# Kernel optimization log

Hardware: AMD Instinct MI355X
Metric: run time of the kernel (lower is better)

Reference implementation:

```python
import jax, jax.numpy as jnp
import numpy as np

B, L, D, H = 8, 1024, 512, 8
DH = D // H
DF = 2048


def setup_inputs() -> dict:
    key = jax.random.key(0)
    ks = jax.random.split(key, 13)
    s = 0.02
    return {
        "hid": jax.random.normal(ks[0], (B, L, D), jnp.float32),
        "img": jax.random.normal(ks[1], (B, L, D), jnp.float32),
        "Wq": s * jax.random.normal(ks[2], (D, D), jnp.float32),
        "Wk": s * jax.random.normal(ks[3], (D, D), jnp.float32),
        "Wv": s * jax.random.normal(ks[4], (D, D), jnp.float32),
        "Wo": s * jax.random.normal(ks[5], (D, D), jnp.float32),
        "Wq2": s * jax.random.normal(ks[6], (D, D), jnp.float32),
        "Wk2": s * jax.random.normal(ks[7], (D, D), jnp.float32),
        "Wv2": s * jax.random.normal(ks[8], (D, D), jnp.float32),
        "Wo2": s * jax.random.normal(ks[9], (D, D), jnp.float32),
        "W1": s * jax.random.normal(ks[10], (D, DF), jnp.float32),
        "W2": s * jax.random.normal(ks[11], (DF, D), jnp.float32),
        "seq": jax.random.randint(ks[12], (B, L), 0, 4),
        "SOC": 3,
        "EOS": 100,
    }


def _ln(x):
    mu = x.mean(-1, keepdims=True)
    v = x.var(-1, keepdims=True)
    return (x - mu) * jax.lax.rsqrt(v + 1e-5)


def _attn(q_in, k_in, v_in, Wq, Wk, Wv, Wo, key_mask=None):
    b, lq, _ = q_in.shape
    q = (q_in @ Wq).reshape(b, lq, H, DH)
    k = (k_in @ Wk).reshape(b, -1, H, DH)
    v = (v_in @ Wv).reshape(b, -1, H, DH)
    scores = jnp.einsum('bqhd,bkhd->bhqk', q, k) * (1.0 / np.sqrt(DH))
    if key_mask is not None:
        scores = jnp.where(key_mask[:, None, None, :], scores, jnp.float32(-1e9))
    a = jax.nn.softmax(scores, axis=-1)
    o = jnp.einsum('bhqk,bkhd->bqhd', a, v).reshape(b, lq, D)
    return o @ Wo


def reference(hid, img, Wq, Wk, Wv, Wo, Wq2, Wk2, Wv2, Wo2, W1, W2, seq, SOC, EOS):
    # cell-start mask: SOC tokens before the first EOS
    soc = (seq == SOC) & (jnp.cumsum(seq == EOS, axis=1) == 0)  # [B,L]
    # stable compaction: True positions first, original order preserved
    order = jnp.argsort(~soc, axis=1, stable=True)              # [B,L]
    ext = jnp.take_along_axis(hid, order[:, :, None], axis=1)   # [B,L,D]
    counts = soc.sum(axis=1)                                    # [B]
    run = jnp.arange(L)[None, :] < counts[:, None]              # [B,L] = extract(soc, soc)
    ext = jnp.where(run[:, :, None], ext, 0.0)                  # zero padding rows (F.pad)
    # Blocks: pre-LN masked self-attn + cross-attn to img + FFN
    x = ext
    xn = _ln(x)
    x = x + _attn(xn, xn, xn, Wq, Wk, Wv, Wo, key_mask=run)
    x = x + _attn(_ln(x), img, img, Wq2, Wk2, Wv2, Wo2)
    x = x + jax.nn.gelu(_ln(x) @ W1) @ W2
    # masked_scatter: write the first `count` rows of x back at soc positions, in order
    inv = jnp.argsort(order, axis=1)
    back = jnp.take_along_axis(x, inv[:, :, None], axis=1)
    hid_new = jnp.where(soc[:, :, None], back, hid)
    return (hid_new, x)
```

## Files before the change

### kernel.cpp

```cpp
#include <hip/hip_runtime.h>
#include <cmath>

#define B 8
#define L 1024
#define D 512
#define H 8
#define DH 64
#define DF 2048
#define BLD (B*L*D)
#define M_TOT (B*L)

typedef __attribute__((ext_vector_type(8))) short bf16x8;
typedef __attribute__((ext_vector_type(4))) float f32x4;
typedef const __attribute__((address_space(1))) void* gas_ptr;
typedef __attribute__((address_space(3))) void* las_ptr;

__device__ __forceinline__ unsigned short f2bf(float f) {
    unsigned int u = __builtin_bit_cast(unsigned int, f);
    u += 0x7FFFu + ((u >> 16) & 1u);
    return (unsigned short)(u >> 16);
}
__device__ __forceinline__ float bf2f(unsigned short s) {
    return __builtin_bit_cast(float, ((unsigned int)s) << 16);
}

__device__ __forceinline__ float gelu_f(float x) {
    float x3 = x * x * x;
    return 0.5f * x * (1.0f + tanhf(0.7978845608028654f * (x + 0.044715f * x3)));
}

__global__ __launch_bounds__(1024) void pos_kernel(const int* __restrict__ seq,
                                                   const int* __restrict__ pSOC,
                                                   const int* __restrict__ pEOS,
                                                   int* __restrict__ pos,
                                                   int* __restrict__ inv,
                                                   int* __restrict__ counts) {
    int b = blockIdx.x, t = threadIdx.x;
    int lane = t & 63, w = t >> 6;
    int sv = seq[b * L + t];
    int SOC = pSOC[0], EOS = pEOS[0];
    int eosf = (sv == EOS) ? 1 : 0;
    unsigned long long em = __ballot(eosf);
    int eexcl = __popcll(em & ((1ull << lane) - 1ull));
    __shared__ int ewt[16], swt[16];
    if (lane == 63) ewt[w] = eexcl + eosf;
    __syncthreads();
    int ebase = 0;
    for (int i = 0; i < w; ++i) ebase += ewt[i];
    int ecum_incl = ebase + eexcl + eosf;
    int socf = (sv == SOC && ecum_incl == 0) ? 1 : 0;
    unsigned long long sm = __ballot(socf);
    int sexcl = __popcll(sm & ((1ull << lane) - 1ull));
    if (lane == 63) swt[w] = sexcl + socf;
    __syncthreads();
    int sbase = 0, stot = 0;
    for (int i = 0; i < 16; ++i) { int v = swt[i]; if (i < w) sbase += v; stot += v; }
    int rank = sbase + sexcl;
    if (socf) pos[b * L + rank] = t;
    inv[b * L + t] = socf ? rank : -1;
    if (t == 0) counts[b] = stot;
}

__global__ void gather_ln(const float* __restrict__ hid, const int* __restrict__ pos,
                          const int* __restrict__ counts,
                          float* __restrict__ X, unsigned short* __restrict__ Y) {
    int j = blockIdx.x % L, b = blockIdx.x / L;
    int cnt = counts[b];
    if ((j & ~127) > cnt) return;
    int t = threadIdx.x;
    float a = 0.f, b2 = 0.f;
    if (j < cnt) {
        const float* src = hid + (size_t)(b * L + pos[b * L + j]) * D;
        a = src[t]; b2 = src[t + 256];
    }
    size_t row = (size_t)(b * L + j);
    X[row * D + t] = a;
    X[row * D + t + 256] = b2;
    float s = a + b2, sq = a * a + b2 * b2;
    for (int m = 1; m < 64; m <<= 1) {
        s += __shfl_xor(s, m);
        sq += __shfl_xor(sq, m);
    }
    __shared__ float ws[4], wq[4];
    int wid = t >> 6;
    if ((t & 63) == 0) { ws[wid] = s; wq[wid] = sq; }
    __syncthreads();
    s = ws[0] + ws[1] + ws[2] + ws[3];
    sq = wq[0] + wq[1] + wq[2] + wq[3];
    float mu = s * (1.0f / D);
    float var = sq * (1.0f / D) - mu * mu;
    float rs = rsqrtf(var + 1e-5f);
    Y[row * D + t] = f2bf((a - mu) * rs);
    Y[row * D + t + 256] = f2bf((b2 - mu) * rs);
}

__global__ void epilogue_kernel(const float* __restrict__ x, const float* __restrict__ hid,
                                const int* __restrict__ inv, const int* __restrict__ counts,
                                float* __restrict__ out0, float* __restrict__ out1) {
    int l = blockIdx.x % L, b = blockIdx.x / L;
    int t = threadIdx.x;
    int cnt = counts[b];
    int r = inv[b * L + l];
    const float4* s0 = (const float4*)((r >= 0 ? x + (size_t)(b * L + r) * D
                                               : hid + (size_t)(b * L + l) * D));
    ((float4*)(out0 + (size_t)(b * L + l) * D))[t] = s0[t];
    int jsrc = l < cnt ? l : cnt;
    const float4* s1 = (const float4*)(x + (size_t)(b * L + jsrc) * D);
    ((float4*)(out1 + (size_t)(b * L + l) * D))[t] = s1[t];
}

__global__ void ln_kernel(const float* __restrict__ X, unsigned short* __restrict__ Y,
                          const int* __restrict__ counts) {
    int row = blockIdx.x;
    if ((row & 1023 & ~127) > counts[row >> 10]) return;
    int t = threadIdx.x;
    const float* xr = X + (size_t)row * D;
    float a = xr[t], b2 = xr[t + 256];
    float s = a + b2, sq = a * a + b2 * b2;
    for (int m = 1; m < 64; m <<= 1) {
        s += __shfl_xor(s, m);
        sq += __shfl_xor(sq, m);
    }
    __shared__ float ws[4], wq[4];
    int wid = t >> 6;
    if ((t & 63) == 0) { ws[wid] = s; wq[wid] = sq; }
    __syncthreads();
    s = ws[0] + ws[1] + ws[2] + ws[3];
    sq = wq[0] + wq[1] + wq[2] + wq[3];
    float mu = s * (1.0f / D);
    float var = sq * (1.0f / D) - mu * mu;
    float rs = rsqrtf(var + 1e-5f);
    Y[(size_t)row * D + t] = f2bf((a - mu) * rs);
    Y[(size_t)row * D + t + 256] = f2bf((b2 - mu) * rs);
}

struct WtArgs {
    const float* src[10];
    unsigned short* dst[10];
    const float* img;
    unsigned short* imgb;
};
__global__ void wtrans_cvt_all(WtArgs a) {
    int bid = blockIdx.x;
    int tx = threadIdx.x, ty = threadIdx.y;
    if (bid >= 4096) {
        int t = ty * 32 + tx;
        int i = (bid - 4096) * 256 + t;
        float4 f = ((const float4*)a.img)[i];
        ushort4 u;
        u.x = f2bf(f.x); u.y = f2bf(f.y); u.z = f2bf(f.z); u.w = f2bf(f.w);
        ((ushort4*)a.imgb)[i] = u;
        return;
    }
    __shared__ float t[32][33];
    int w, tn, tk, K, N;
    if (bid < 2048)      { w = bid >> 8;      int t2 = bid & 255;  N = 512;  K = 512;  tn = t2 & 15; tk = t2 >> 4; }
    else if (bid < 3072) { w = 8;             int t2 = bid - 2048; N = 2048; K = 512;  tn = t2 & 63; tk = t2 >> 6; }
    else                 { w = 9;             int t2 = bid - 3072; N = 512;  K = 2048; tn = t2 & 15; tk = t2 >> 4; }
    const float* W = a.src[w];
    unsigned short* Wt = a.dst[w];
    int k0 = tk * 32, n0 = tn * 32;
    for (int i = ty; i < 32; i += 8)
        t[i][tx] = W[(size_t)(k0 + i) * N + n0 + tx];
    __syncthreads();
    for (int i = ty; i < 32; i += 8)
        Wt[(size_t)(n0 + i) * K + k0 + tx] = f2bf(t[tx][i]);
}

template<bool SKIP>
__global__ __launch_bounds__(256) void vtrans_kernel(const unsigned short* __restrict__ V,
                                                     int vstride,
                                                     unsigned short* __restrict__ Vt,
                                                     const int* __restrict__ counts) {
    __shared__ unsigned short t[64][72];
    int l0 = (blockIdx.x & 15) * 64;
    int h = (blockIdx.x >> 4) & 7;
    int b = blockIdx.x >> 7;
    if (SKIP && l0 > counts[b]) return;
    int tid = threadIdx.x;
    const unsigned short* vb = V + (size_t)b * L * vstride + h * DH;
    for (int e = tid; e < 512; e += 256) {
        int i = e >> 3, d0 = (e & 7) * 8;
        *(bf16x8*)&t[i][d0] = *(const bf16x8*)&vb[(size_t)(l0 + i) * vstride + d0];
    }
    __syncthreads();
    for (int e = tid; e < 512; e += 256) {
        int d = e & 63, i0 = (e >> 6) * 8;
        bf16x8 val;
        #pragma unroll
        for (int j = 0; j < 8; ++j) val[j] = t[i0 + j][d];
        *(bf16x8*)&Vt[((size_t)((b * H + h) * DH + d)) * L + l0 + i0] = val;
    }
}

template<int MODE, bool SKIP, int S>
__global__ __launch_bounds__(256) void gemm_mfma(const unsigned short* __restrict__ A,
                                                 const unsigned short* __restrict__ Wt,
                                                 void* __restrict__ Cv,
                                                 int K, int N,
                                                 const int* __restrict__ counts) {
    int m0 = blockIdx.y * 64, n0 = blockIdx.x * 128;
    if (SKIP && (m0 & 1023) > counts[m0 >> 10]) return;
    int Kc = K / S;
    int kbeg = blockIdx.z * Kc;
    int nk = Kc / 64;
    __shared__ __align__(16) unsigned short As[3][64 * 64];
    __shared__ __align__(16) unsigned short Bs[3][128 * 64];
    int tid = threadIdx.x, lane = tid & 63, wid = tid >> 6;
    int wm = (wid >> 1) * 32, wn = (wid & 1) * 64;
    int r16 = lane & 15, g = lane >> 4;
    f32x4 acc[2][4] = {};

#define STAGE(bufi, kt) do {                                                          \
    int kk_ = kbeg + (kt) * 64;                                                       \
    _Pragma("unroll")                                                                 \
    for (int q_ = 0; q_ < 2; ++q_) {                                                  \
        int e_ = q_ * 256 + tid;                                                      \
        int r_ = e_ >> 3, c_ = ((e_ & 7) ^ (r_ & 7)) * 8;                             \
        __builtin_amdgcn_global_load_lds((gas_ptr)(A + (size_t)(m0 + r_) * K + kk_ + c_), \
                                         (las_ptr)(&As[bufi][0] + (size_t)e_ * 8), 16, 0, 0); \
    }                                                                                 \
    _Pragma("unroll")                                                                 \
    for (int q_ = 0; q_ < 4; ++q_) {                                                  \
        int e_ = q_ * 256 + tid;                                                      \
        int r_ = e_ >> 3, c_ = ((e_ & 7) ^ (r_ & 7)) * 8;                             \
        __builtin_amdgcn_global_load_lds((gas_ptr)(Wt + (size_t)(n0 + r_) * K + kk_ + c_), \
                                         (las_ptr)(&Bs[bufi][0] + (size_t)e_ * 8), 16, 0, 0); \
    }                                                                                 \
} while (0)

    STAGE(0, 0);
    if (nk > 1) STAGE(1, 1);
    asm volatile("s_waitcnt vmcnt(6)" ::: "memory");
    __builtin_amdgcn_s_barrier();
    __builtin_amdgcn_sched_barrier(0);
    int swz = (r16 & 7) * 8;
    for (int kt = 0; kt < nk; ++kt) {
        int cur = kt % 3;
        if (kt + 2 < nk) STAGE((kt + 2) % 3, kt + 2);
        #pragma unroll
        for (int ks = 0; ks < 2; ++ks) {
            bf16x8 av[2], bv[4];
            #pragma unroll
            for (int m = 0; m < 2; ++m)
                av[m] = *(const bf16x8*)&As[cur][(wm + m * 16 + r16) * 64 + ((ks * 32 + g * 8) ^ swz)];
            #pragma unroll
            for (int n = 0; n < 4; ++n)
                bv[n] = *(const bf16x8*)&Bs[cur][(wn + n * 16 + r16) * 64 + ((ks * 32 + g * 8) ^ swz)];
            #pragma unroll
            for (int m = 0; m < 2; ++m)
                #pragma unroll
                for (int n = 0; n < 4; ++n)
                    acc[m][n] = __builtin_amdgcn_mfma_f32_16x16x32_bf16(av[m], bv[n], acc[m][n], 0, 0, 0);
        }
        if (kt + 2 < nk) asm volatile("s_waitcnt vmcnt(6)" ::: "memory");
        else             asm volatile("s_waitcnt vmcnt(0)" ::: "memory");
        __builtin_amdgcn_s_barrier();
        __builtin_amdgcn_sched_barrier(0);
    }
#undef STAGE
    #pragma unroll
    for (int m = 0; m < 2; ++m)
        #pragma unroll
        for (int n = 0; n < 4; ++n)
            #pragma unroll
            for (int r = 0; r < 4; ++r) {
                int grow = m0 + wm + m * 16 + g * 4 + r;
                int gcol = n0 + wn + n * 16 + r16;
                size_t off = (size_t)grow * N + gcol;
                float vv = acc[m][n][r];
                if (MODE == 1) {
                    if (S > 1) atomicAdd((float*)Cv + off, vv);
                    else ((float*)Cv)[off] += vv;
                }
                else if (MODE == 2) ((unsigned short*)Cv)[off] = f2bf(gelu_f(vv));
                else ((unsigned short*)Cv)[off] = f2bf(vv);
            }
}

template<int MODE, bool SKIP, int S>
__global__ __launch_bounds__(256) void gemm_mfma128(const unsigned short* __restrict__ A,
                                                    const unsigned short* __restrict__ Wt,
                                                    void* __restrict__ Cv,
                                                    int K, int N,
                                                    const int* __restrict__ counts) {
    int m0 = blockIdx.y * 128, n0 = blockIdx.x * 128;
    if (SKIP && (m0 & 1023) > counts[m0 >> 10]) return;
    int Kc = K / S;
    int kbeg = blockIdx.z * Kc;
    int nk = Kc / 64;
    __shared__ __align__(16) unsigned short As[2][128 * 64];
    __shared__ __align__(16) unsigned short Bs[2][128 * 64];
    int tid = threadIdx.x, lane = tid & 63, wid = tid >> 6;
    int wm = (wid >> 1) * 64, wn = (wid & 1) * 64;
    int r16 = lane & 15, g = lane >> 4;
    f32x4 acc[4][4] = {};

#define STAGE(bufi, kt) do {                                                          \
    int kk_ = kbeg + (kt) * 64;                                                       \
    _Pragma("unroll")                                                                 \
    for (int q_ = 0; q_ < 4; ++q_) {                                                  \
        int e_ = q_ * 256 + tid;                                                      \
        int r_ = e_ >> 3, c_ = ((e_ & 7) ^ (r_ & 7)) * 8;                             \
        __builtin_amdgcn_global_load_lds((gas_ptr)(A + (size_t)(m0 + r_) * K + kk_ + c_), \
                                         (las_ptr)(&As[bufi][0] + (size_t)e_ * 8), 16, 0, 0); \
        __builtin_amdgcn_global_load_lds((gas_ptr)(Wt + (size_t)(n0 + r_) * K + kk_ + c_), \
                                         (las_ptr)(&Bs[bufi][0] + (size_t)e_ * 8), 16, 0, 0); \
    }                                                                                 \
} while (0)

    STAGE(0, 0);
    if (nk > 1) STAGE(1, 1);
    asm volatile("s_waitcnt vmcnt(8)" ::: "memory");
    __builtin_amdgcn_s_barrier();
    __builtin_amdgcn_sched_barrier(0);
    int swz = (r16 & 7) * 8;
    for (int kt = 0; kt < nk; ++kt) {
        int cur = kt & 1;
        #pragma unroll
        for (int ks = 0; ks < 2; ++ks) {
            bf16x8 av[4], bv[4];
            #pragma unroll
            for (int m = 0; m < 4; ++m)
                av[m] = *(const bf16x8*)&As[cur][(wm + m * 16 + r16) * 64 + ((ks * 32 + g * 8) ^ swz)];
            #pragma unroll
            for (int n = 0; n < 4; ++n)
                bv[n] = *(const bf16x8*)&Bs[cur][(wn + n * 16 + r16) * 64 + ((ks * 32 + g * 8) ^ swz)];
            #pragma unroll
            for (int m = 0; m < 4; ++m)
                #pragma unroll
                for (int n = 0; n < 4; ++n)
                    acc[m][n] = __builtin_amdgcn_mfma_f32_16x16x32_bf16(av[m], bv[n], acc[m][n], 0, 0, 0);
        }
        __builtin_amdgcn_s_barrier();
        if (kt + 2 < nk) STAGE(cur, kt + 2);
        if (kt + 1 < nk) {
            if (kt + 2 < nk) asm volatile("s_waitcnt vmcnt(8)" ::: "memory");
            else             asm volatile("s_waitcnt vmcnt(0)" ::: "memory");
        }
        __builtin_amdgcn_s_barrier();
        __builtin_amdgcn_sched_barrier(0);
    }
#undef STAGE
    #pragma unroll
    for (int m = 0; m < 4; ++m)
        #pragma unroll
        for (int n = 0; n < 4; ++n)
            #pragma unroll
            for (int r = 0; r < 4; ++r) {
                int grow = m0 + wm + m * 16 + g * 4 + r;
                int gcol = n0 + wn + n * 16 + r16;
                size_t off = (size_t)grow * N + gcol;
                float vv = acc[m][n][r];
                if (MODE == 1) {
                    if (S > 1) atomicAdd((float*)Cv + off, vv);
                    else ((float*)Cv)[off] += vv;
                }
                else if (MODE == 2) ((unsigned short*)Cv)[off] = f2bf(gelu_f(vv));
                else ((unsigned short*)Cv)[off] = f2bf(vv);
            }
}

template<bool MASK, bool SPLIT>
__global__ __launch_bounds__(256) void attn_mfma(const unsigned short* __restrict__ Q, int qstride,
                                                 const unsigned short* __restrict__ Kb, int kstride,
                                                 const unsigned short* __restrict__ Vt,
                                                 unsigned short* __restrict__ O,
                                                 unsigned short* __restrict__ PO,
                                                 float* __restrict__ ML,
                                                 const int* __restrict__ counts) {
    int nwg = gridDim.x;
    int wg = (blockIdx.x & 7) * (nwg >> 3) + (blockIdx.x >> 3);
    int qt = wg & 15;
    int cidx = SPLIT ? ((wg >> 4) & 1) : 0;
    int h = SPLIT ? ((wg >> 5) & 7) : ((wg >> 4) & 7);
    int b = SPLIT ? (wg >> 8) : (wg >> 7);
    int cntb = counts[b];
    if (qt * 64 > cntb) return;
    __shared__ __align__(16) unsigned short Ks[64][64];
    __shared__ __align__(16) unsigned short Vs[64][64];
    __shared__ __align__(16) unsigned short Ps[4][16][64];
    int tid = threadIdx.x, lane = tid & 63, wid = tid >> 6;
    int q0 = qt * 64 + wid * 16;
    int cnt = MASK ? cntb : L;
    int nt = MASK ? min(16, max(1, (cnt + 63) >> 6)) : 16;
    int kt0 = SPLIT ? cidx * 8 : 0;
    int kt1 = SPLIT ? (cidx * 8 + 8) : nt;
    int r16 = lane & 15, g = lane >> 4;
    int swmask = (r16 & 7) << 3;
    const unsigned short* qbase = Q + ((size_t)(b * L + q0 + r16) * qstride + h * DH + g * 8);
    bf16x8 qv0 = *(const bf16x8*)(qbase);
    bf16x8 qv1 = *(const bf16x8*)(qbase + 32);
    f32x4 o_acc[4] = {};
    float m_run[4], l_run[4];
    #pragma unroll
    for (int r = 0; r < 4; ++r) { m_run[r] = -1e30f; l_run[r] = 0.f; }
    const unsigned short* kb = Kb + (size_t)b * L * kstride + h * DH;
    const unsigned short* vtb = Vt + (size_t)(b * H + h) * DH * L;
    bf16x8 kreg[2], vreg[2];
    #pragma unroll
    for (int q = 0; q < 2; ++q) {
        int e = q * 256 + tid, kv = e >> 3, c0 = (e & 7) * 8;
        kreg[q] = *(const bf16x8*)&kb[(size_t)(kt0 * 64 + kv) * kstride + c0];
        vreg[q] = *(const bf16x8*)&vtb[(size_t)kv * L + kt0 * 64 + c0];
    }
    for (int kt = kt0; kt < kt1; ++kt) {
        __syncthreads();
        #pragma unroll
        for (int q = 0; q < 2; ++q) {
            int e = q * 256 + tid, kv = e >> 3, c0 = (e & 7) * 8;
            int sw = c0 ^ ((kv & 7) << 3);
            *(bf16x8*)&Ks[kv][sw] = kreg[q];
            *(bf16x8*)&Vs[kv][sw] = vreg[q];
        }
        __syncthreads();
        if (kt + 1 < kt1) {
            #pragma unroll
            for (int q = 0; q < 2; ++q) {
                int e = q * 256 + tid, kv = e >> 3, c0 = (e & 7) * 8;
                kreg[q] = *(const bf16x8*)&kb[(size_t)((kt + 1) * 64 + kv) * kstride + c0];
                vreg[q] = *(const bf16x8*)&vtb[(size_t)kv * L + (kt + 1) * 64 + c0];
            }
        }
        f32x4 s[4];
        #pragma unroll
        for (int n = 0; n < 4; ++n) {
            bf16x8 k0 = *(const bf16x8*)&Ks[n * 16 + r16][(g * 8) ^ swmask];
            bf16x8 k1 = *(const bf16x8*)&Ks[n * 16 + r16][(g * 8 + 32) ^ swmask];
            f32x4 z = {};
            z = __builtin_amdgcn_mfma_f32_16x16x32_bf16(qv0, k0, z, 0, 0, 0);
            s[n] = __builtin_amdgcn_mfma_f32_16x16x32_bf16(qv1, k1, z, 0, 0, 0);
        }
        #pragma unroll
        for (int n = 0; n < 4; ++n)
            #pragma unroll
            for (int r = 0; r < 4; ++r) {
                float v = s[n][r] * 0.125f;
                if (MASK) {
                    int kidx = kt * 64 + n * 16 + r16;
                    v = (kidx < cnt) ? v : -1e30f;
                }
                s[n][r] = v;
            }
        #pragma unroll
        for (int r = 0; r < 4; ++r) {
            float rm = fmaxf(fmaxf(s[0][r], s[1][r]), fmaxf(s[2][r], s[3][r]));
            #pragma unroll
            for (int mm = 1; mm < 16; mm <<= 1) rm = fmaxf(rm, __shfl_xor(rm, mm));
            float m_new = fmaxf(m_run[r], rm);
            float rs = 0.f;
            #pragma unroll
            for (int n = 0; n < 4; ++n) { float e = __expf(s[n][r] - m_new); s[n][r] = e; rs += e; }
            #pragma unroll
            for (int mm = 1; mm < 16; mm <<= 1) rs += __shfl_xor(rs, mm);
            float factor = __expf(m_run[r] - m_new);
            l_run[r] = l_run[r] * factor + rs;
            m_run[r] = m_new;
            #pragma unroll
            for (int n = 0; n < 4; ++n) o_acc[n][r] *= factor;
        }
        #pragma unroll
        for (int n = 0; n < 4; ++n)
            #pragma unroll
            for (int r = 0; r < 4; ++r) {
                int qrow = g * 4 + r;
                Ps[wid][qrow][(n * 16 + r16) ^ ((qrow & 7) << 3)] = f2bf(s[n][r]);
            }
        bf16x8 pa0 = *(const bf16x8*)&Ps[wid][r16][(g * 8) ^ swmask];
        bf16x8 pa1 = *(const bf16x8*)&Ps[wid][r16][(g * 8 + 32) ^ swmask];
        #pragma unroll
        for (int n = 0; n < 4; ++n) {
            bf16x8 v0 = *(const bf16x8*)&Vs[n * 16 + r16][(g * 8) ^ swmask];
            bf16x8 v1 = *(const bf16x8*)&Vs[n * 16 + r16][(g * 8 + 32) ^ swmask];
            o_acc[n] = __builtin_amdgcn_mfma_f32_16x16x32_bf16(pa0, v0, o_acc[n], 0, 0, 0);
            o_acc[n] = __builtin_amdgcn_mfma_f32_16x16x32_bf16(pa1, v1, o_acc[n], 0, 0, 0);
        }
    }
    #pragma unroll
    for (int r = 0; r < 4; ++r) {
        float inv = 1.0f / l_run[r];
        int row = q0 + g * 4 + r;
        if (SPLIT) {
            size_t basec = (((size_t)cidx * B + b) * H + h) * L + row;
            #pragma unroll
            for (int n = 0; n < 4; ++n)
                PO[basec * DH + n * 16 + r16] = f2bf(o_acc[n][r] * inv);
            if (r16 == 0) { ML[basec * 2] = m_run[r]; ML[basec * 2 + 1] = l_run[r]; }
        } else {
            size_t ro = (size_t)(b * L + row) * D + h * DH;
            #pragma unroll
            for (int n = 0; n < 4; ++n)
                O[ro + n * 16 + r16] = f2bf(o_acc[n][r] * inv);
        }
    }
}

__global__ __launch_bounds__(256) void attn_merge(const unsigned short* __restrict__ PO,
                                                  const float* __restrict__ ML,
                                                  unsigned short* __restrict__ O,
                                                  const int* __restrict__ counts) {
    int qt = blockIdx.x & 15, h = (blockIdx.x >> 4) & 7, b = blockIdx.x >> 7;
    if (qt * 64 > counts[b]) return;
    int tid = threadIdx.x;
    int row = qt * 64 + (tid >> 2);
    int d0 = (tid & 3) * 16;
    size_t base = (size_t)(b * H + h) * L + row;
    size_t cstride = (size_t)B * H * L;
    float m0 = ML[base * 2], l0 = ML[base * 2 + 1];
    float m1 = ML[(base + cstride) * 2], l1 = ML[(base + cstride) * 2 + 1];
    float M = fmaxf(m0, m1);
    float w0 = __expf(m0 - M) * l0, w1 = __expf(m1 - M) * l1;
    float inv = 1.0f / (w0 + w1);
    w0 *= inv; w1 *= inv;
    const bf16x8* p0 = (const bf16x8*)&PO[base * DH + d0];
    const bf16x8* p1 = (const bf16x8*)&PO[(base + cstride) * DH + d0];
    unsigned short* op = O + ((size_t)(b * L + row) * D + h * DH + d0);
    #pragma unroll
    for (int q = 0; q < 2; ++q) {
        bf16x8 a = p0[q], c = p1[q], r;
        #pragma unroll
        for (int j = 0; j < 8; ++j)
            r[j] = (short)f2bf(bf2f((unsigned short)a[j]) * w0 + bf2f((unsigned short)c[j]) * w1);
        *(bf16x8*)(op + q * 8) = r;
    }
}

extern "C" void kernel_launch(void* const* d_in, const int* in_sizes, int n_in,
                              void* d_out, int out_size, void* d_ws, size_t ws_size,
                              hipStream_t stream) {
    const float* hid = (const float*)d_in[0];
    const float* img = (const float*)d_in[1];
    const int* seq   = (const int*)d_in[12];
    const int* pSOC  = (const int*)d_in[13];
    const int* pEOS  = (const int*)d_in[14];
    float* out0 = (float*)d_out;
    float* out1 = out0 + (size_t)BLD;

    char* w = (char*)d_ws;
    int* pos    = (int*)w;
    int* inv    = pos + B * L;
    int* counts = inv + B * L;
    size_t off = 128 * 1024;
    float* x = (float*)(w + off);                     off += (size_t)BLD * 4;
    unsigned short* qkv = (unsigned short*)(w + off); off += (size_t)M_TOT * 3 * D * 2;
    unsigned short* o   = (unsigned short*)(w + off); off += (size_t)BLD * 2;
    unsigned short* vt  = (unsigned short*)(w + off); off += (size_t)BLD * 2;
    unsigned short* xn  = (unsigned short*)(w + off); off += (size_t)BLD * 2;
    unsigned short* imgb= (unsigned short*)(w + off); off += (size_t)BLD * 2;
    unsigned short* Wqt  = (unsigned short*)(w + off); off += (size_t)D * D * 2;
    unsigned short* Wkt  = (unsigned short*)(w + off); off += (size_t)D * D * 2;
    unsigned short* Wvt  = (unsigned short*)(w + off); off += (size_t)D * D * 2;
    unsigned short* Wot  = (unsigned short*)(w + off); off += (size_t)D * D * 2;
    unsigned short* Wq2t = (unsigned short*)(w + off); off += (size_t)D * D * 2;
    unsigned short* Wk2t = (unsigned short*)(w + off); off += (size_t)D * D * 2;
    unsigned short* Wv2t = (unsigned short*)(w + off); off += (size_t)D * D * 2;
    unsigned short* Wo2t = (unsigned short*)(w + off); off += (size_t)D * D * 2;
    unsigned short* W1t  = (unsigned short*)(w + off); off += (size_t)D * DF * 2;
    unsigned short* W2t  = (unsigned short*)(w + off); off += (size_t)D * DF * 2;
    float* ml            = (float*)(w + off);          off += (size_t)2 * B * H * L * 2 * 4;
    unsigned short* q2  = qkv;
    unsigned short* kv2 = qkv + (size_t)M_TOT * D;
    unsigned short* mid = qkv;
    unsigned short* po  = xn;

    pos_kernel<<<B, 1024, 0, stream>>>(seq, pSOC, pEOS, pos, inv, counts);
    WtArgs wa;
    wa.src[0] = (const float*)d_in[2];  wa.dst[0] = Wqt;
    wa.src[1] = (const float*)d_in[3];  wa.dst[1] = Wkt;
    wa.src[2] = (const float*)d_in[4];  wa.dst[2] = Wvt;
    wa.src[3] = (const float*)d_in[5];  wa.dst[3] = Wot;
    wa.src[4] = (const float*)d_in[6];  wa.dst[4] = Wq2t;
    wa.src[5] = (const float*)d_in[7];  wa.dst[5] = Wk2t;
    wa.src[6] = (const float*)d_in[8];  wa.dst[6] = Wv2t;
    wa.src[7] = (const float*)d_in[9];  wa.dst[7] = Wo2t;
    wa.src[8] = (const float*)d_in[10]; wa.dst[8] = W1t;
    wa.src[9] = (const float*)d_in[11]; wa.dst[9] = W2t;
    wa.img = img; wa.imgb = imgb;
    wtrans_cvt_all<<<8192, dim3(32, 8), 0, stream>>>(wa);

    int attn_grid = B * H * (L / 64);
    gather_ln<<<B * L, 256, 0, stream>>>(hid, pos, counts, x, xn);
    gemm_mfma128<3, true, 1><<<dim3(12, 64, 1), 256, 0, stream>>>(xn, Wqt, qkv, D, 3 * D, counts);
    vtrans_kernel<true><<<attn_grid, 256, 0, stream>>>(qkv + 2 * D, 3 * D, vt, counts);
    attn_mfma<true, false><<<attn_grid, 256, 0, stream>>>(qkv, 3 * D, qkv + D, 3 * D, vt, o, po, ml, counts);
    gemm_mfma<1, true, 4><<<dim3(4, 128, 4), 256, 0, stream>>>(o, Wot, x, D, D, counts);
    ln_kernel<<<M_TOT, 256, 0, stream>>>(x, xn, counts);
    gemm_mfma128<3, false, 1><<<dim3(8, 64, 1), 256, 0, stream>>>(imgb, Wk2t, kv2, D, 2 * D, counts);
    gemm_mfma<3, true, 1><<<dim3(4, 128, 1), 256, 0, stream>>>(xn, Wq2t, q2, D, D, counts);
    vtrans_kernel<false><<<attn_grid, 256, 0, stream>>>(kv2 + D, 2 * D, vt, counts);
    attn_mfma<false, true><<<attn_grid * 2, 256, 0, stream>>>(q2, D, kv2, 2 * D, vt, o, po, ml, counts);
    attn_merge<<<attn_grid, 256, 0, stream>>>(po, ml, o, counts);
    gemm_mfma<1, true, 4><<<dim3(4, 128, 4), 256, 0, stream>>>(o, Wo2t, x, D, D, counts);
    ln_kernel<<<M_TOT, 256, 0, stream>>>(x, xn, counts);
    gemm_mfma128<2, true, 1><<<dim3(16, 64, 1), 256, 0, stream>>>(xn, W1t, mid, D, DF, counts);
    gemm_mfma128<1, true, 4><<<dim3(4, 64, 4), 256, 0, stream>>>(mid, W2t, x, DF, D, counts);
    epilogue_kernel<<<B * L, 128, 0, stream>>>(x, hid, inv, counts, out0, out1);
}
```

Before: 232.8 us.

## Replace multi-buffered GEMM kernels with single-buffer K=32 unified GEMM body

Merges the two GEMM kernels into one templated body parameterised by M tile size. The K step drops from 64 to 32, and the triple/double-buffered async LDS staging with explicit vmcnt waits becomes a single buffer guarded by __syncthreads. This uses less LDS, which could allow more resident blocks, but it gives up the overlap of global loads with MFMA compute and doubles the number of barrier iterations.

```diff
diff --git a/kernel.cpp b/kernel.cpp
--- a/kernel.cpp
+++ b/kernel.cpp
@@ -193,172 +193,78 @@
     }
 }
 
-template<int MODE, bool SKIP, int S>
-__global__ __launch_bounds__(256) void gemm_mfma(const unsigned short* __restrict__ A,
-                                                 const unsigned short* __restrict__ Wt,
-                                                 void* __restrict__ Cv,
-                                                 int K, int N,
-                                                 const int* __restrict__ counts) {
-    int m0 = blockIdx.y * 64, n0 = blockIdx.x * 128;
-    if (SKIP && (m0 & 1023) > counts[m0 >> 10]) return;
-    int Kc = K / S;
-    int kbeg = blockIdx.z * Kc;
-    int nk = Kc / 64;
-    __shared__ __align__(16) unsigned short As[3][64 * 64];
-    __shared__ __align__(16) unsigned short Bs[3][128 * 64];
-    int tid = threadIdx.x, lane = tid & 63, wid = tid >> 6;
-    int wm = (wid >> 1) * 32, wn = (wid & 1) * 64;
+template<int MODE, int TM, int S>
+__device__ __forceinline__ void gemm_body(const unsigned short* __restrict__ A,
+                                          const unsigned short* __restrict__ Wt,
+                                          void* __restrict__ Cv,
+                                          int K, int N, int m0, int n0, int kbeg, int nk,
+                                          unsigned short* As, unsigned short* Bs, int tid) {
+    int lane = tid & 63, wid = tid >> 6;
+    int wm = (wid >> 1) * (TM / 2), wn = (wid & 1) * 64;
     int r16 = lane & 15, g = lane >> 4;
-    f32x4 acc[2][4] = {};
-
-#define STAGE(bufi, kt) do {                                                          \
-    int kk_ = kbeg + (kt) * 64;                                                       \
-    _Pragma("unroll")                                                                 \
-    for (int q_ = 0; q_ < 2; ++q_) {                                                  \
-        int e_ = q_ * 256 + tid;                                                      \
-        int r_ = e_ >> 3, c_ = ((e_ & 7) ^ (r_ & 7)) * 8;                             \
-        __builtin_amdgcn_global_load_lds((gas_ptr)(A + (size_t)(m0 + r_) * K + kk_ + c_), \
-                                         (las_ptr)(&As[bufi][0] + (size_t)e_ * 8), 16, 0, 0); \
-    }                                                                                 \
-    _Pragma("unroll")                                                                 \
-    for (int q_ = 0; q_ < 4; ++q_) {                                                  \
-        int e_ = q_ * 256 + tid;                                                      \
-        int r_ = e_ >> 3, c_ = ((e_ & 7) ^ (r_ & 7)) * 8;                             \
-        __builtin_amdgcn_global_load_lds((gas_ptr)(Wt + (size_t)(n0 + r_) * K + kk_ + c_), \
-                                         (las_ptr)(&Bs[bufi][0] + (size_t)e_ * 8), 16, 0, 0); \
-    }                                                                                 \
-} while (0)
-
-    STAGE(0, 0);
-    if (nk > 1) STAGE(1, 1);
-    asm volatile("s_waitcnt vmcnt(6)" ::: "memory");
-    __builtin_amdgcn_s_barrier();
-    __builtin_amdgcn_sched_barrier(0);
-    int swz = (r16 & 7) * 8;
+    constexpr int MR = TM / 32;
+    f32x4 acc[MR][4] = {};
+    int sx = (r16 & 3) ^ ((r16 >> 2) & 3);
+    int koff = (g ^ sx) * 8;
     for (int kt = 0; kt < nk; ++kt) {
-        int cur = kt % 3;
-        if (kt + 2 < nk) STAGE((kt + 2) % 3, kt + 2);
-        #pragma unroll
-        for (int ks = 0; ks < 2; ++ks) {
-            bf16x8 av[2], bv[4];
-            #pragma unroll
-            for (int m = 0; m < 2; ++m)
-                av[m] = *(const bf16x8*)&As[cur][(wm + m * 16 + r16) * 64 + ((ks * 32 + g * 8) ^ swz)];
+        int kk = kbeg + kt * 32;
+        #pragma unroll
+        for (int q = 0; q < TM / 64; ++q) {
+            int e = q * 256 + tid;
+            int r = e >> 2, c = ((e & 3) ^ (r & 3) ^ ((r >> 2) & 3)) * 8;
+            __builtin_amdgcn_global_load_lds((gas_ptr)(A + (size_t)(m0 + r) * K + kk + c),
+                                             (las_ptr)(As + e * 8), 16, 0, 0);
+        }
+        #pragma unroll
+        for (int q = 0; q < 2; ++q) {
+            int e = q * 256 + tid;
+            int r = e >> 2, c = ((e & 3) ^ (r & 3) ^ ((r >> 2) & 3)) * 8;
+            __builtin_amdgcn_global_load_lds((gas_ptr)(Wt + (size_t)(n0 + r) * K + kk + c),
+                                             (las_ptr)(Bs + e * 8), 16, 0, 0);
+        }
+        __syncthreads();
+        bf16x8 av[MR], bv[4];
+        #pragma unroll
+        for (int m = 0; m < MR; ++m) av[m] = *(const bf16x8*)&As[(wm + m * 16 + r16) * 32 + koff];
+        #pragma unroll
+        for (int n = 0; n < 4; ++n) bv[n] = *(const bf16x8*)&Bs[(wn + n * 16 + r16) * 32 + koff];
+        #pragma unroll
+        for (int m = 0; m < MR; ++m)
             #pragma unroll
             for (int n = 0; n < 4; ++n)
-                bv[n] = *(const bf16x8*)&Bs[cur][(wn + n * 16 + r16) * 64 + ((ks * 32 + g * 8) ^ swz)];
-            #pragma unroll
-            for (int m = 0; m < 2; ++m)
-                #pragma unroll
-                for (int n = 0; n < 4; ++n)
-                    acc[m][n] = __builtin_amdgcn_mfma_f32_16x16x32_bf16(av[m], bv[n], acc[m][n], 0, 0, 0);
-        }
-        if (kt + 2 < nk) asm volatile("s_waitcnt vmcnt(6)" ::: "memory");
-        else             asm volatile("s_waitcnt vmcnt(0)" ::: "memory");
-        __builtin_amdgcn_s_barrier();
-        __builtin_amdgcn_sched_barrier(0);
-    }
-#undef STAGE
+                acc[m][n] = __builtin_amdgcn_mfma_f32_16x16x32_bf16(av[m], bv[n], acc[m][n], 0, 0, 0);
+        __syncthreads();
+    }
     #pragma unroll
-    for (int m = 0; m < 2; ++m)
+    for (int m = 0; m < MR; ++m)
         #pragma unroll
         for (int n = 0; n < 4; ++n)
             #pragma unroll
             for (int r = 0; r < 4; ++r) {
                 int grow = m0 + wm + m * 16 + g * 4 + r;
                 int gcol = n0 + wn + n * 16 + r16;
-                size_t off = (size_t)grow * N + gcol;
+                size_t off2 = (size_t)grow * N + gcol;
                 float vv = acc[m][n][r];
                 if (MODE == 1) {
-                    if (S > 1) atomicAdd((float*)Cv + off, vv);
-                    else ((float*)Cv)[off] += vv;
+                    if (S > 1) atomicAdd((float*)Cv + off2, vv);
+                    else ((float*)Cv)[off2] += vv;
                 }
-                else if (MODE == 2) ((unsigned short*)Cv)[off] = f2bf(gelu_f(vv));
-                else ((unsigned short*)Cv)[off] = f2bf(vv);
+                else if (MODE == 2) ((unsigned short*)Cv)[off2] = f2bf(gelu_f(vv));
+                else ((unsigned short*)Cv)[off2] = f2bf(vv);
             }
 }
 
-template<int MODE, bool SKIP, int S>
-__global__ __launch_bounds__(256) void gemm_mfma128(const unsigned short* __restrict__ A,
-                                                    const unsigned short* __restrict__ Wt,
-                                                    void* __restrict__ Cv,
-                                                    int K, int N,
-                                                    const int* __restrict__ counts) {
-    int m0 = blockIdx.y * 128, n0 = blockIdx.x * 128;
+template<int MODE, int TM, bool SKIP, int S>
+__global__ __launch_bounds__(256) void gemm_k(const unsigned short* __restrict__ A,
+                                              const unsigned short* __restrict__ Wt,
+                                              void* __restrict__ Cv,
+                                              int K, int N, const int* __restrict__ counts) {
+    int m0 = blockIdx.y * TM, n0 = blockIdx.x * 128;
     if (SKIP && (m0 & 1023) > counts[m0 >> 10]) return;
-    int Kc = K / S;
-    int kbeg = blockIdx.z * Kc;
-    int nk = Kc / 64;
-    __shared__ __align__(16) unsigned short As[2][128 * 64];
-    __shared__ __align__(16) unsigned short Bs[2][128 * 64];
-    int tid = threadIdx.x, lane = tid & 63, wid = tid >> 6;
-    int wm = (wid >> 1) * 64, wn = (wid & 1) * 64;
-    int r16 = lane & 15, g = lane >> 4;
-    f32x4 acc[4][4] = {};
-
-#define STAGE(bufi, kt) do {                                                          \
-    int kk_ = kbeg + (kt) * 64;                                                       \
-    _Pragma("unroll")                                                                 \
-    for (int q_ = 0; q_ < 4; ++q_) {                                                  \
-        int e_ = q_ * 256 + tid;                                                      \
-        int r_ = e_ >> 3, c_ = ((e_ & 7) ^ (r_ & 7)) * 8;                             \
-        __builtin_amdgcn_global_load_lds((gas_ptr)(A + (size_t)(m0 + r_) * K + kk_ + c_), \
-                                         (las_ptr)(&As[bufi][0] + (size_t)e_ * 8), 16, 0, 0); \
-        __builtin_amdgcn_global_load_lds((gas_ptr)(Wt + (size_t)(n0 + r_) * K + kk_ + c_), \
-                                         (las_ptr)(&Bs[bufi][0] + (size_t)e_ * 8), 16, 0, 0); \
-    }                                                                                 \
-} while (0)
-
-    STAGE(0, 0);
-    if (nk > 1) STAGE(1, 1);
-    asm volatile("s_waitcnt vmcnt(8)" ::: "memory");
-    __builtin_amdgcn_s_barrier();
-    __builtin_amdgcn_sched_barrier(0);
-    int swz = (r16 & 7) * 8;
-    for (int kt = 0; kt < nk; ++kt) {
-        int cur = kt & 1;
-        #pragma unroll
-        for (int ks = 0; ks < 2; ++ks) {
-            bf16x8 av[4], bv[4];
-            #pragma unroll
-            for (int m = 0; m < 4; ++m)
-                av[m] = *(const bf16x8*)&As[cur][(wm + m * 16 + r16) * 64 + ((ks * 32 + g * 8) ^ swz)];
-            #pragma unroll
-            for (int n = 0; n < 4; ++n)
-                bv[n] = *(const bf16x8*)&Bs[cur][(wn + n * 16 + r16) * 64 + ((ks * 32 + g * 8) ^ swz)];
-            #pragma unroll
-            for (int m = 0; m < 4; ++m)
-                #pragma unroll
-                for (int n = 0; n < 4; ++n)
-                    acc[m][n] = __builtin_amdgcn_mfma_f32_16x16x32_bf16(av[m], bv[n], acc[m][n], 0, 0, 0);
-        }
-        __builtin_amdgcn_s_barrier();
-        if (kt + 2 < nk) STAGE(cur, kt + 2);
-        if (kt + 1 < nk) {
-            if (kt + 2 < nk) asm volatile("s_waitcnt vmcnt(8)" ::: "memory");
-            else             asm volatile("s_waitcnt vmcnt(0)" ::: "memory");
-        }
-        __builtin_amdgcn_s_barrier();
-        __builtin_amdgcn_sched_barrier(0);
-    }
-#undef STAGE
-    #pragma unroll
-    for (int m = 0; m < 4; ++m)
-        #pragma unroll
-        for (int n = 0; n < 4; ++n)
-            #pragma unroll
-            for (int r = 0; r < 4; ++r) {
-                int grow = m0 + wm + m * 16 + g * 4 + r;
-                int gcol = n0 + wn + n * 16 + r16;
-                size_t off = (size_t)grow * N + gcol;
-                float vv = acc[m][n][r];
-                if (MODE == 1) {
-                    if (S > 1) atomicAdd((float*)Cv + off, vv);
-                    else ((float*)Cv)[off] += vv;
-                }
-                else if (MODE == 2) ((unsigned short*)Cv)[off] = f2bf(gelu_f(vv));
-                else ((unsigned short*)Cv)[off] = f2bf(vv);
-            }
+    int Kc = K / S, kbeg = blockIdx.z * Kc, nk = Kc / 32;
+    __shared__ __align__(16) unsigned short As[TM * 32];
+    __shared__ __align__(16) unsigned short Bs[128 * 32];
+    gemm_body<MODE, TM, S>(A, Wt, Cv, K, N, m0, n0, kbeg, nk, As, Bs, threadIdx.x);
 }
 
 template<bool MASK, bool SPLIT>
@@ -580,19 +486,19 @@
 
     int attn_grid = B * H * (L / 64);
     gather_ln<<<B * L, 256, 0, stream>>>(hid, pos, counts, x, xn);
-    gemm_mfma128<3, true, 1><<<dim3(12, 64, 1), 256, 0, stream>>>(xn, Wqt, qkv, D, 3 * D, counts);
+    gemm_k<3, 128, true, 1><<<dim3(12, 64, 1), 256, 0, stream>>>(xn, Wqt, qkv, D, 3 * D, counts);
     vtrans_kernel<true><<<attn_grid, 256, 0, stream>>>(qkv + 2 * D, 3 * D, vt, counts);
     attn_mfma<true, false><<<attn_grid, 256, 0, stream>>>(qkv, 3 * D, qkv + D, 3 * D, vt, o, po, ml, counts);
-    gemm_mfma<1, true, 4><<<dim3(4, 128, 4), 256, 0, stream>>>(o, Wot, x, D, D, counts);
+    gemm_k<1, 64, true, 4><<<dim3(4, 128, 4), 256, 0, stream>>>(o, Wot, x, D, D, counts);
     ln_kernel<<<M_TOT, 256, 0, stream>>>(x, xn, counts);
-    gemm_mfma128<3, false, 1><<<dim3(8, 64, 1), 256, 0, stream>>>(imgb, Wk2t, kv2, D, 2 * D, counts);
-    gemm_mfma<3, true, 1><<<dim3(4, 128, 1), 256, 0, stream>>>(xn, Wq2t, q2, D, D, counts);
+    gemm_k<3, 128, false, 1><<<dim3(8, 64, 1), 256, 0, stream>>>(imgb, Wk2t, kv2, D, 2 * D, counts);
+    gemm_k<3, 64, true, 1><<<dim3(4, 128, 1), 256, 0, stream>>>(xn, Wq2t, q2, D, D, counts);
     vtrans_kernel<false><<<attn_grid, 256, 0, stream>>>(kv2 + D, 2 * D, vt, counts);
     attn_mfma<false, true><<<attn_grid * 2, 256, 0, stream>>>(q2, D, kv2, 2 * D, vt, o, po, ml, counts);
     attn_merge<<<attn_grid, 256, 0, stream>>>(po, ml, o, counts);
-    gemm_mfma<1, true, 4><<<dim3(4, 128, 4), 256, 0, stream>>>(o, Wo2t, x, D, D, counts);
+    gemm_k<1, 64, true, 4><<<dim3(4, 128, 4), 256, 0, stream>>>(o, Wo2t, x, D, D, counts);
     ln_kernel<<<M_TOT, 256, 0, stream>>>(x, xn, counts);
-    gemm_mfma128<2, true, 1><<<dim3(16, 64, 1), 256, 0, stream>>>(xn, W1t, mid, D, DF, counts);
-    gemm_mfma128<1, true, 4><<<dim3(4, 64, 4), 256, 0, stream>>>(mid, W2t, x, DF, D, counts);
+    gemm_k<2, 128, true, 1><<<dim3(16, 64, 1), 256, 0, stream>>>(xn, W1t, mid, D, DF, counts);
+    gemm_k<1, 128, true, 4><<<dim3(4, 64, 4), 256, 0, stream>>>(mid, W2t, x, DF, D, counts);
     epilogue_kernel<<<B * L, 128, 0, stream>>>(x, hid, inv, counts, out0, out1);
 }
```

New measurement: 256.6 us. +10.2%, slower.
